# Kernel tuning notes

Measured on AMD Instinct MI355X. Metric: run time of the kernel, lower is better.

The kernel has to match this reference:

```python
import jax, jax.numpy as jnp
import numpy as np

H, W = 256, 512
SCORE_THR = 0.2
NMS_THR = 0.15
TOPK = 4096


def _make_anchors():
    xs = (np.arange(W) + 0.5) * 0.4 - 0.2 * W
    ys = (np.arange(H) + 0.5) * 0.4 - 0.2 * H
    gx, gy = np.meshgrid(xs, ys)            # [H, W]
    anc = np.zeros((H, W, 2, 7), dtype=np.float32)
    anc[..., 0] = gx[..., None]
    anc[..., 1] = gy[..., None]
    anc[..., 2] = -1.0
    anc[..., 3] = 1.56  # h
    anc[..., 4] = 1.6   # w
    anc[..., 5] = 3.9   # l
    anc[..., 0, 6] = 0.0
    anc[..., 1, 6] = np.pi / 2
    return jnp.asarray(anc)


def _make_T(theta, tx, ty, tz):
    c, s = np.cos(theta), np.sin(theta)
    T = np.eye(4, dtype=np.float32)
    T[0, 0], T[0, 1], T[1, 0], T[1, 1] = c, -s, s, c
    T[0, 3], T[1, 3], T[2, 3] = tx, ty, tz
    return jnp.asarray(T)


def setup_inputs() -> dict:
    key = jax.random.key(0)
    k1, k2, k3, k4 = jax.random.split(key, 4)
    return {
        "anchors": _make_anchors(),
        "psm_v": jax.random.normal(k1, (1, 2, H, W), jnp.float32),
        "rm_v": jax.random.normal(k2, (1, 14, H, W), jnp.float32) * 0.1,
        "psm_i": jax.random.normal(k3, (1, 2, H, W), jnp.float32),
        "rm_i": jax.random.normal(k4, (1, 14, H, W), jnp.float32) * 0.1,
        "t_proj": _make_T(0.05, 2.0, -1.0, 0.1),
        "t_ego": _make_T(-0.1, 5.0, 3.0, 0.0),
    }


def delta_to_boxes3d(rm, anchors):
    # rm: [1, 14, H, W] -> [A, 7]; anchors: [H, W, 2, 7] xyzhwlr -> [A, 7]
    d = jnp.transpose(rm[0], (1, 2, 0)).reshape(-1, 7)
    a = anchors.reshape(-1, 7)
    ad = jnp.sqrt(a[:, 4] ** 2 + a[:, 5] ** 2)          # diag of w,l
    xy = d[:, :2] * ad[:, None] + a[:, :2]
    z = d[:, 2] * a[:, 3] + a[:, 2]
    dims = jnp.exp(d[:, 3:6]) * a[:, 3:6]               # h, w, l
    yaw = d[:, 6] + a[:, 6]
    return jnp.concatenate([xy, z[:, None], dims, yaw[:, None]], axis=1)


def boxes_to_corners_3d(b):
    # b: [N, 7] x,y,z,h,w,l,yaw (order 'hwl') -> [N, 8, 3]
    h, w, l, yaw = b[:, 3], b[:, 4], b[:, 5], b[:, 6]
    sx = jnp.array([1, 1, -1, -1, 1, 1, -1, -1], jnp.float32) * 0.5
    sy = jnp.array([1, -1, -1, 1, 1, -1, -1, 1], jnp.float32) * 0.5
    sz = jnp.array([-1, -1, -1, -1, 1, 1, 1, 1], jnp.float32) * 0.5
    x = l[:, None] * sx
    y = w[:, None] * sy
    z = h[:, None] * sz
    c, s = jnp.cos(yaw)[:, None], jnp.sin(yaw)[:, None]
    xr = x * c - y * s + b[:, 0:1]
    yr = x * s + y * c + b[:, 1:2]
    zr = z + b[:, 2:3]
    return jnp.stack([xr, yr, zr], axis=-1)


def project_box3d(corners, T):
    # corners: [N, 8, 3]; T: [4, 4]
    return jnp.einsum('ij,nkj->nki', T[:3, :3], corners) + T[:3, 3]


def corner_to_center(corners):
    # inverse of boxes_to_corners_3d, order 'hwl'
    xyz = corners.mean(axis=1)
    h = corners[:, 4:, 2].mean(axis=1) - corners[:, :4, 2].mean(axis=1)
    dl = corners[:, (0, 1, 4, 5), :2] - corners[:, (3, 2, 7, 6), :2]
    dw = corners[:, (0, 3, 4, 7), :2] - corners[:, (1, 2, 5, 6), :2]
    l = jnp.linalg.norm(dl, axis=-1).mean(axis=1)
    w = jnp.linalg.norm(dw, axis=-1).mean(axis=1)
    d = dl.sum(axis=1)
    yaw = jnp.arctan2(d[:, 1], d[:, 0])
    return jnp.concatenate(
        [xyz, h[:, None], w[:, None], l[:, None], yaw[:, None]], axis=1)


def standup_boxes(corners):
    # [N, 8, 3] -> [N, 4] x1,y1,x2,y2 over BEV
    mn = corners[..., :2].min(axis=1)
    mx = corners[..., :2].max(axis=1)
    return jnp.concatenate([mn, mx], axis=1)


def iou_matrix(b):
    area = (b[:, 2] - b[:, 0]) * (b[:, 3] - b[:, 1])
    lt = jnp.maximum(b[:, None, :2], b[None, :, :2])
    rb = jnp.minimum(b[:, None, 2:], b[None, :, 2:])
    wh = jnp.clip(rb - lt, 0.0)
    inter = wh[..., 0] * wh[..., 1]
    return inter / (area[:, None] + area[None, :] - inter + 1e-6)


def nms_keep(iou, valid, thresh):
    K = iou.shape[0]
    idx = jnp.arange(K)

    def body(i, keep):
        sup = (iou[i] > thresh) & (idx > i) & keep[i]
        return keep & ~sup

    return jax.lax.fori_loop(0, K, body, valid)


def _branch(psm, rm, anchors):
    scores = jax.nn.sigmoid(jnp.transpose(psm[0], (1, 2, 0))).reshape(-1)
    boxes = delta_to_boxes3d(rm, anchors)
    return boxes, scores


def reference(anchors, psm_v, rm_v, psm_i, rm_i, t_proj, t_ego):
    boxes_v, scores_v = _branch(psm_v, rm_v, anchors)
    boxes_i, scores_i = _branch(psm_i, rm_i, anchors)
    # project infra branch boxes into ego frame via corner transform
    corners_i = boxes_to_corners_3d(boxes_i)
    boxes_i = corner_to_center(project_box3d(corners_i, t_proj))
    boxes = jnp.concatenate([boxes_v, boxes_i], axis=0)       # [2A, 7]
    scores = jnp.concatenate([scores_v, scores_i], axis=0)    # [2A]
    # project all to ego space
    proj = project_box3d(boxes_to_corners_3d(boxes), t_ego)   # [2A, 8, 3]
    # static replacement of masked_select: mask + top-K
    masked = jnp.where(scores > SCORE_THR, scores, -1.0)
    top_s, top_i = jax.lax.top_k(masked, TOPK)
    corners_k = proj[top_i]                                    # [K, 8, 3]
    iou = iou_matrix(standup_boxes(corners_k))
    keep = nms_keep(iou, top_s > SCORE_THR, NMS_THR)
    final = top_s * keep.astype(top_s.dtype)
    # pack corners + surviving scores: [K, 25]
    return jnp.concatenate([corners_k.reshape(TOPK, 24), final[:, None]], axis=1)
```

## Files before the change

kernel.cpp:

```cpp
#include <hip/hip_runtime.h>
#include <stdint.h>

typedef unsigned int u32;
typedef unsigned long long u64;

#define HH 256
#define WW 512
#define HW (HH*WW)
#define N2 (2*HW)
#define NT (2*N2)
#define TOPK 4096
#define SCORE_THR 0.2f
#define NMS_THR 0.15f

#define OFF_KEYS   0ull
#define OFF_GHIST  ((size_t)NT*4)
#define OFF_GHIST2 (OFF_GHIST + 4096)
#define OFF_CNT    (OFF_GHIST2 + 4096)
#define OFF_VALIDM (OFF_CNT + 16)
#define OFF_CAND   (OFF_VALIDM + 512)
#define OFF_STAND  OFF_CAND
#define OFF_SELIDX (OFF_CAND + 65536)
#define OFF_SELSC  (OFF_SELIDX + (size_t)TOPK*4)
#define OFF_TDIAG  (OFF_SELSC + (size_t)TOPK*4)
#define ZERO_BYTES (4096 + 4096 + 16)
#define RANK_J 8

#define SLOT8 4160

__device__ __forceinline__ u32 f2ord(float f) {
    u32 b = __float_as_uint(f);
    return (b & 0x80000000u) ? ~b : (b | 0x80000000u);
}

__global__ void __launch_bounds__(1024) k_keys(const float* __restrict__ psm_v,
                                               const float* __restrict__ psm_i,
                                               u32* __restrict__ keys,
                                               u32* __restrict__ ghist) {
    __shared__ u32 lh[1024];
    int t = threadIdx.x;
    lh[t] = 0;
    __syncthreads();
    int n = blockIdx.x * 1024 + t;
    int br = n >> 18;
    int m  = n & (N2 - 1);
    int a  = m & 1;
    int hw = m >> 1;
    const float* psm = br ? psm_i : psm_v;
    float x = psm[a * HW + hw];
    float s = 1.0f / (1.0f + __builtin_expf(-x));
    u32 key = 0u;
    if (s > SCORE_THR) key = f2ord(s);
    keys[n] = key;
    if (key) atomicAdd(&lh[key >> 22], 1u);
    __syncthreads();
    u32 c = lh[t];
    if (c) atomicAdd(&ghist[t], c);
}

__device__ __forceinline__ void pivot1024(const u32* __restrict__ arr, u32 target,
                                          u32* out_bin, u32* out_next, int l) {
    u32 h[16], loc[16];
#pragma unroll
    for (int j = 0; j < 16; ++j) h[j] = arr[l * 16 + j];
    loc[15] = h[15];
#pragma unroll
    for (int j = 14; j >= 0; --j) loc[j] = loc[j + 1] + h[j];
    u32 T = loc[0];
    u32 incl = T;
#pragma unroll
    for (int d = 1; d < 64; d <<= 1) {
        u32 v = __shfl_down(incl, d);
        if (l + d < 64) incl += v;
    }
    u32 E = incl - T;
#pragma unroll
    for (int j = 0; j < 16; ++j) {
        u32 S  = loc[j] + E;
        u32 Sn = (j < 15 ? loc[j + 1] : 0u) + E;
        if (S >= target && Sn < target) {
            *out_bin = (u32)(l * 16 + j);
            *out_next = Sn;
        }
    }
}

__global__ void __launch_bounds__(1024) k_hist2(const u32* __restrict__ ghist,
                                                const u32* __restrict__ keys,
                                                u32* __restrict__ ghist2) {
    __shared__ u32 lh[1024];
    __shared__ u32 b1_sh;
    int tid = threadIdx.x;
    lh[tid] = 0;
    if (tid < 64) {
        u32 bin = 0xFFFFFFFFu, nxt = 0;
        pivot1024(ghist, (u32)TOPK, &bin, &nxt, tid);
        if (bin != 0xFFFFFFFFu) b1_sh = bin;
    }
    __syncthreads();
    u32 b1 = b1_sh;
    int n = blockIdx.x * 1024 + tid;
    u32 key = keys[n];
    if ((key >> 22) == b1) atomicAdd(&lh[(key >> 12) & 1023u], 1u);
    __syncthreads();
    u32 c = lh[tid];
    if (c) atomicAdd(&ghist2[tid], c);
}

__global__ void __launch_bounds__(1024) k_collect(const u32* __restrict__ ghist,
                                                  const u32* __restrict__ ghist2,
                                                  const u32* __restrict__ keys,
                                                  u64* __restrict__ cand,
                                                  u32* __restrict__ cnt) {
    __shared__ u32 b1_sh, t2_sh, b2_sh;
    int tid = threadIdx.x;
    if (tid < 64) {
        u32 bin = 0xFFFFFFFFu, nxt = 0;
        pivot1024(ghist, (u32)TOPK, &bin, &nxt, tid);
        if (bin != 0xFFFFFFFFu) { b1_sh = bin; t2_sh = (u32)TOPK - nxt; }
    }
    __syncthreads();
    if (tid < 64) {
        u32 bin = 0xFFFFFFFFu, nxt = 0;
        pivot1024(ghist2, t2_sh, &bin, &nxt, tid);
        if (bin != 0xFFFFFFFFu) b2_sh = bin;
    }
    __syncthreads();
    u32 thr20 = (b1_sh << 10) | b2_sh;
    int n = blockIdx.x * 1024 + tid;
    u32 key = keys[n];
    if ((key >> 12) >= thr20) {
        u32 pos = atomicAdd(cnt, 1u);
        if (pos < 8192u)
            cand[pos] = ((u64)key << 32) | (u64)(u32)(~(u32)n);
    }
}

__global__ void __launch_bounds__(256) k_rank1(const u64* __restrict__ cand,
                                               const u32* __restrict__ cnt,
                                               u32* __restrict__ partial) {
    __shared__ u64 tile[1024];
    int tid = threadIdx.x;
    int i = blockIdx.x * 256 + tid;
    u32 base = blockIdx.y * 1024u;
    u32 c = *cnt;
    if (c > 8192u) c = 8192u;
    u64 my = (i < (int)c) ? cand[i] : 0ull;
#pragma unroll
    for (int k = 0; k < 4; ++k) {
        u32 idx = base + tid + k * 256;
        tile[tid + k * 256] = (idx < c) ? cand[idx] : 0ull;
    }
    __syncthreads();
    u32 lim = (c > base) ? ((c - base < 1024u) ? (c - base) : 1024u) : 0u;
    u32 r = 0;
#pragma unroll 4
    for (u32 k = 0; k < lim; ++k) r += (tile[k] > my) ? 1u : 0u;
    partial[blockIdx.y * 8192 + i] = r;
}

__global__ void __launch_bounds__(256) k_scatter(const u64* __restrict__ cand,
                                                 const u32* __restrict__ cnt,
                                                 const u32* __restrict__ partial,
                                                 u32* __restrict__ sel_idx) {
    int i = blockIdx.x * 256 + threadIdx.x;
    u32 c = *cnt;
    if (c > 8192u) c = 8192u;
    if (i >= (int)c) return;
    u32 rank = 0;
#pragma unroll
    for (int bj = 0; bj < RANK_J; ++bj) rank += partial[bj * 8192 + i];
    if (rank < (u32)TOPK) {
        u64 my = cand[i];
        sel_idx[rank] = ~((u32)(my & 0xFFFFFFFFull));
    }
}

__device__ __forceinline__ void box_corners(const float b[7], float cx[8], float cy[8], float cz[8]) {
    const float sx[8] = {0.5f,0.5f,-0.5f,-0.5f,0.5f,0.5f,-0.5f,-0.5f};
    const float sy[8] = {0.5f,-0.5f,-0.5f,0.5f,0.5f,-0.5f,-0.5f,0.5f};
    const float sz[8] = {-0.5f,-0.5f,-0.5f,-0.5f,0.5f,0.5f,0.5f,0.5f};
    float c = __builtin_cosf(b[6]), s = __builtin_sinf(b[6]);
#pragma unroll
    for (int k = 0; k < 8; k++) {
        float x = b[5] * sx[k], y = b[4] * sy[k], z = b[3] * sz[k];
        cx[k] = x * c - y * s + b[0];
        cy[k] = x * s + y * c + b[1];
        cz[k] = z + b[2];
    }
}

__device__ __forceinline__ void proj_T(const float* __restrict__ T, float cx[8], float cy[8], float cz[8]) {
#pragma unroll
    for (int k = 0; k < 8; k++) {
        float x = cx[k], y = cy[k], z = cz[k];
        cx[k] = T[0] * x + T[1] * y + T[2]  * z + T[3];
        cy[k] = T[4] * x + T[5] * y + T[6]  * z + T[7];
        cz[k] = T[8] * x + T[9] * y + T[10] * z + T[11];
    }
}

__device__ __forceinline__ void corner_to_center(const float cx[8], const float cy[8], const float cz[8], float b[7]) {
    float mx = 0.f, my = 0.f, mz = 0.f;
#pragma unroll
    for (int k = 0; k < 8; k++) { mx += cx[k]; my += cy[k]; mz += cz[k]; }
    mx *= 0.125f; my *= 0.125f; mz *= 0.125f;
    float htop = (cz[4] + cz[5] + cz[6] + cz[7]) * 0.25f;
    float hbot = (cz[0] + cz[1] + cz[2] + cz[3]) * 0.25f;
    const int lA[4] = {0,1,4,5}, lB[4] = {3,2,7,6};
    const int wA[4] = {0,3,4,7}, wB[4] = {1,2,5,6};
    float l = 0.f, w = 0.f, dx = 0.f, dy = 0.f;
#pragma unroll
    for (int i = 0; i < 4; i++) {
        float ax = cx[lA[i]] - cx[lB[i]];
        float ay = cy[lA[i]] - cy[lB[i]];
        l += __builtin_sqrtf(ax * ax + ay * ay);
        dx += ax; dy += ay;
    }
#pragma unroll
    for (int i = 0; i < 4; i++) {
        float ax = cx[wA[i]] - cx[wB[i]];
        float ay = cy[wA[i]] - cy[wB[i]];
        w += __builtin_sqrtf(ax * ax + ay * ay);
    }
    b[0] = mx; b[1] = my; b[2] = mz;
    b[3] = htop - hbot;
    b[4] = w * 0.25f;
    b[5] = l * 0.25f;
    b[6] = atan2f(dy, dx);
}

__global__ void __launch_bounds__(256) k_boxes(const float* __restrict__ anchors,
                                               const float* __restrict__ psm_v,
                                               const float* __restrict__ psm_i,
                                               const float* __restrict__ rm_v,
                                               const float* __restrict__ rm_i,
                                               const float* __restrict__ tproj,
                                               const float* __restrict__ tego,
                                               const u32* __restrict__ sel_idx,
                                               float* __restrict__ sel_sc,
                                               float* __restrict__ out,
                                               float4* __restrict__ stand,
                                               u64* __restrict__ validm) {
    int k = blockIdx.x * blockDim.x + threadIdx.x;
    if (k >= TOPK) return;
    int n = (int)(sel_idx[k] & (u32)(NT - 1));
    int br = n >> 18;
    int m  = n & (N2 - 1);
    int a  = m & 1;
    int hw = m >> 1;

    const float* psm = br ? psm_i : psm_v;
    float xs = psm[a * HW + hw];
    float s  = 1.0f / (1.0f + __builtin_expf(-xs));
    sel_sc[k] = (s > SCORE_THR) ? s : -1.0f;
    u64 vbits = __ballot(s > SCORE_THR);
    if ((threadIdx.x & 63) == 0) validm[k >> 6] = vbits;

    const float* rm = br ? rm_i : rm_v;
    float d[7];
#pragma unroll
    for (int j = 0; j < 7; j++) d[j] = rm[(a * 7 + j) * HW + hw];
    const float* anc = anchors + (size_t)m * 7;
    float a0 = anc[0], a1 = anc[1], a2 = anc[2], a3 = anc[3], a4 = anc[4], a5 = anc[5], a6 = anc[6];
    float ad = __builtin_sqrtf(a4 * a4 + a5 * a5);
    float b[7];
    b[0] = d[0] * ad + a0;
    b[1] = d[1] * ad + a1;
    b[2] = d[2] * a3 + a2;
    b[3] = __builtin_expf(d[3]) * a3;
    b[4] = __builtin_expf(d[4]) * a4;
    b[5] = __builtin_expf(d[5]) * a5;
    b[6] = d[6] + a6;

    if (br) {
        float cx[8], cy[8], cz[8];
        box_corners(b, cx, cy, cz);
        proj_T(tproj, cx, cy, cz);
        corner_to_center(cx, cy, cz, b);
    }

    float cx[8], cy[8], cz[8];
    box_corners(b, cx, cy, cz);
    proj_T(tego, cx, cy, cz);

    float mnx = cx[0], mny = cy[0], mxx = cx[0], mxy = cy[0];
#pragma unroll
    for (int c = 0; c < 8; c++) {
        out[(size_t)k * 25 + c * 3 + 0] = cx[c];
        out[(size_t)k * 25 + c * 3 + 1] = cy[c];
        out[(size_t)k * 25 + c * 3 + 2] = cz[c];
        mnx = fminf(mnx, cx[c]); mny = fminf(mny, cy[c]);
        mxx = fmaxf(mxx, cx[c]); mxy = fmaxf(mxy, cy[c]);
    }
    stand[k] = make_float4(mnx, mny, mxx, mxy);
}

__global__ void __launch_bounds__(256) k_mask(const float4* __restrict__ stand,
                                              u64* __restrict__ mask) {
    int i = blockIdx.x * 4 + (threadIdx.x >> 6);
    int t = threadIdx.x & 63;
    int w0 = i >> 6;
    float4 bi = stand[i];
    float areai = (bi.z - bi.x) * (bi.w - bi.y);
    u64 myword = 0ull;
    for (int w = w0; w < 64; ++w) {
        int j = w * 64 + t;
        float4 bj = stand[j];
        float areaj = (bj.z - bj.x) * (bj.w - bj.y);
        float ltx = fmaxf(bi.x, bj.x), lty = fmaxf(bi.y, bj.y);
        float rbx = fminf(bi.z, bj.z), rby = fminf(bi.w, bj.w);
        float iw = fmaxf(rbx - ltx, 0.0f), ih = fmaxf(rby - lty, 0.0f);
        float inter = iw * ih;
        float iou = inter / (areai + areaj - inter + 1e-6f);
        bool sup = (iou > NMS_THR) && (j > i);
        u64 bits = __ballot(sup);
        if (t == w) myword = bits;
    }
    mask[(size_t)i * 64 + t] = myword;
}

__global__ void __launch_bounds__(64) k_diag(const float4* __restrict__ stand,
                                             u64* __restrict__ tdiag) {
    __shared__ float4 sb[64];
    int B = blockIdx.x, l = threadIdx.x;
    float4 me = stand[B * 64 + l];
    sb[l] = me;
    __syncthreads();
    float aream = (me.z - me.x) * (me.w - me.y);
    u64 T = 0ull;
    for (int j = 0; j < 64; ++j) {
        float4 bj = sb[j];
        float areaj = (bj.z - bj.x) * (bj.w - bj.y);
        float ltx = fmaxf(bj.x, me.x), lty = fmaxf(bj.y, me.y);
        float rbx = fminf(bj.z, me.z), rby = fminf(bj.w, me.w);
        float iw = fmaxf(rbx - ltx, 0.0f), ih = fmaxf(rby - lty, 0.0f);
        float inter = iw * ih;
        float iou = inter / (areaj + aream - inter + 1e-6f);
        bool sup = (iou > NMS_THR) && (j < l);
        T |= sup ? (1ull << j) : 0ull;
    }
    tdiag[B * 64 + l] = T;
}

__device__ __forceinline__ u64 readlane64(u64 v, int lane) {
    u32 lo = (u32)__builtin_amdgcn_readlane((int)(u32)v, lane);
    u32 hi = (u32)__builtin_amdgcn_readlane((int)(u32)(v >> 32), lane);
    return ((u64)hi << 32) | (u64)lo;
}

__device__ __forceinline__ void nms_stage8(const u64* __restrict__ mask,
                                           const u64* __restrict__ tdiag,
                                           int c, int l, u64* wb) {
    bool act = (2 * (l & 31) + 1) >= c;
    const u64* gb = mask + (size_t)c * 4096 + (size_t)l * 2;
    if (act) {
#pragma unroll
        for (int k = 0; k < 32; ++k) {
            __builtin_amdgcn_global_load_lds(
                (const __attribute__((address_space(1))) void*)(gb + (size_t)k * 128),
                (__attribute__((address_space(3))) void*)(wb + (size_t)k * 128), 16, 0, 0);
        }
    }
    if (l < 32) {
        __builtin_amdgcn_global_load_lds(
            (const __attribute__((address_space(1))) void*)(tdiag + (size_t)c * 64 + (size_t)l * 2),
            (__attribute__((address_space(3))) void*)(wb + 4096), 16, 0, 0);
    }
}

__global__ void __launch_bounds__(64, 1)
k_nms(const u64* __restrict__ mask,
      const u64* __restrict__ tdiag,
      const u64* __restrict__ validm,
      const float* __restrict__ sc,
      float* __restrict__ out) {
    __shared__ u64 ring[3 * SLOT8];
    int l = threadIdx.x;
    u64 remv = 0ull;
    u64 keep = 0ull;
    u64 vreg = validm[l];

    nms_stage8(mask, tdiag, 0, l, ring);
    nms_stage8(mask, tdiag, 1, l, ring + SLOT8);

    for (int B = 0; B < 64; ++B) {
        int s = B % 3;
        u64* wb = ring + (size_t)s * SLOT8;
        if (B == 63) __builtin_amdgcn_s_waitcnt(0x0F70);
        else         __builtin_amdgcn_s_waitcnt(0x8F71);
        __builtin_amdgcn_sched_barrier(0);
        __asm__ volatile("" ::: "memory");
        u64 Tl = wb[4096 + l];
        if (B + 2 < 64)
            nms_stage8(mask, tdiag, B + 2, l, ring + (size_t)((B + 2) % 3) * SLOT8);
        u64 curw = readlane64(remv, B);
        u64 vm = readlane64(vreg, B);
        u64 ve = vm & ~curw;
        u64 D = 0ull, P = ve;
        while (D != P) {
            u64 nD = ve & ~__ballot((Tl & P) != 0ull);
            u64 nP = ve & ~__ballot((Tl & nD) != 0ull);
            D = nD; P = nP;
        }
        u64 kb = D;
        keep = (l == B) ? kb : keep;
        u32 klo = (u32)__builtin_amdgcn_readfirstlane((int)(u32)kb);
        u32 khi = (u32)__builtin_amdgcn_readfirstlane((int)(u32)(kb >> 32));
        u64 p = 0ull;
#pragma unroll
        for (int g = 0; g < 8; ++g) {
            u32 bits = ((g < 4 ? klo : khi) >> ((g & 3) * 8)) & 0xFFu;
            if (bits) {
#pragma unroll
                for (int k = 0; k < 8; ++k) {
                    u64 row = wb[(size_t)(g * 8 + k) * 64 + l];
                    p |= row & (0ull - (u64)((bits >> k) & 1u));
                }
            }
        }
        remv |= p;
    }

    for (int c = 0; c < 64; ++c) {
        u64 kc = readlane64(keep, c);
        float s = sc[c * 64 + l];
        out[(size_t)(c * 64 + l) * 25 + 24] = ((kc >> l) & 1ull) ? s : 0.0f;
    }
}

extern "C" void kernel_launch(void* const* d_in, const int* in_sizes, int n_in,
                              void* d_out, int out_size, void* d_ws, size_t ws_size,
                              hipStream_t stream) {
    const float* anchors = (const float*)d_in[0];
    const float* psm_v   = (const float*)d_in[1];
    const float* rm_v    = (const float*)d_in[2];
    const float* psm_i   = (const float*)d_in[3];
    const float* rm_i    = (const float*)d_in[4];
    const float* tproj   = (const float*)d_in[5];
    const float* tego    = (const float*)d_in[6];
    float* out = (float*)d_out;
    char* ws = (char*)d_ws;

    u32*    keys    = (u32*)(ws + OFF_KEYS);
    u64*    mask    = (u64*)(ws + OFF_KEYS);
    u32*    partial = (u32*)(ws + OFF_KEYS);
    u32*    ghist   = (u32*)(ws + OFF_GHIST);
    u32*    ghist2  = (u32*)(ws + OFF_GHIST2);
    u32*    cnt     = (u32*)(ws + OFF_CNT);
    u64*    validm  = (u64*)(ws + OFF_VALIDM);
    u64*    cand    = (u64*)(ws + OFF_CAND);
    float4* stand   = (float4*)(ws + OFF_STAND);
    u32*    sel_idx = (u32*)(ws + OFF_SELIDX);
    float*  sel_sc  = (float*)(ws + OFF_SELSC);
    u64*    tdiag   = (u64*)(ws + OFF_TDIAG);

    hipMemsetAsync(ws + OFF_GHIST, 0, ZERO_BYTES, stream);
    k_keys   <<<NT / 1024, 1024, 0, stream>>>(psm_v, psm_i, keys, ghist);
    k_hist2  <<<NT / 1024, 1024, 0, stream>>>(ghist, keys, ghist2);
    k_collect<<<NT / 1024, 1024, 0, stream>>>(ghist, ghist2, keys, cand, cnt);
    k_rank1  <<<dim3(32, RANK_J), 256, 0, stream>>>(cand, cnt, partial);
    k_scatter<<<32, 256, 0, stream>>>(cand, cnt, partial, sel_idx);
    k_boxes  <<<TOPK / 256, 256, 0, stream>>>(anchors, psm_v, psm_i, rm_v, rm_i,
                                              tproj, tego, sel_idx, sel_sc, out,
                                              stand, validm);
    k_mask   <<<TOPK / 4, 256, 0, stream>>>(stand, mask);
    k_diag   <<<64, 64, 0, stream>>>(stand, tdiag);
    k_nms    <<<1, 64, 0, stream>>>(mask, tdiag, validm, sel_sc, out);
}
```

Baseline: 287.7 us.

## Split serial NMS across 64 blocks with flag-based inter-block publishing

Replaces the single-wavefront NMS, which walked all 64 column blocks serially with an LDS prefetch ring, by 64 blocks, one per 64-box column block. Each block preloads its mask column into LDS, then spins on per-block keep words published in global memory by the earlier blocks. It ORs in their suppression, resolves its own diagonal block, and publishes its keep mask. This aims to overlap the mask loading across CUs and shorten the serial chain. The cost is cross-block spin-waiting on relaxed atomics, which relies on all 64 blocks being resident at once and on the published values becoming visible without fences.

```diff
diff --git a/kernel.cpp b/kernel.cpp
--- a/kernel.cpp
+++ b/kernel.cpp
@@ -17,16 +17,15 @@
 #define OFF_GHIST  ((size_t)NT*4)
 #define OFF_GHIST2 (OFF_GHIST + 4096)
 #define OFF_CNT    (OFF_GHIST2 + 4096)
-#define OFF_VALIDM (OFF_CNT + 16)
+#define OFF_PUB    (OFF_CNT + 16)
+#define OFF_VALIDM (OFF_PUB + 2048)
 #define OFF_CAND   (OFF_VALIDM + 512)
 #define OFF_STAND  OFF_CAND
 #define OFF_SELIDX (OFF_CAND + 65536)
 #define OFF_SELSC  (OFF_SELIDX + (size_t)TOPK*4)
 #define OFF_TDIAG  (OFF_SELSC + (size_t)TOPK*4)
-#define ZERO_BYTES (4096 + 4096 + 16)
+#define ZERO_BYTES (4096 + 4096 + 16 + 2048)
 #define RANK_J 8
-
-#define SLOT8 4160
 
 __device__ __forceinline__ u32 f2ord(float f) {
     u32 b = __float_as_uint(f);
@@ -349,84 +348,75 @@
     return ((u64)hi << 32) | (u64)lo;
 }
 
-__device__ __forceinline__ void nms_stage8(const u64* __restrict__ mask,
-                                           const u64* __restrict__ tdiag,
-                                           int c, int l, u64* wb) {
-    bool act = (2 * (l & 31) + 1) >= c;
-    const u64* gb = mask + (size_t)c * 4096 + (size_t)l * 2;
-    if (act) {
-#pragma unroll
-        for (int k = 0; k < 32; ++k) {
-            __builtin_amdgcn_global_load_lds(
-                (const __attribute__((address_space(1))) void*)(gb + (size_t)k * 128),
-                (__attribute__((address_space(3))) void*)(wb + (size_t)k * 128), 16, 0, 0);
-        }
-    }
-    if (l < 32) {
-        __builtin_amdgcn_global_load_lds(
-            (const __attribute__((address_space(1))) void*)(tdiag + (size_t)c * 64 + (size_t)l * 2),
-            (__attribute__((address_space(3))) void*)(wb + 4096), 16, 0, 0);
-    }
-}
-
 __global__ void __launch_bounds__(64, 1)
 k_nms(const u64* __restrict__ mask,
       const u64* __restrict__ tdiag,
       const u64* __restrict__ validm,
       const float* __restrict__ sc,
+      u64* pub,
       float* __restrict__ out) {
-    __shared__ u64 ring[3 * SLOT8];
+    __shared__ u64 colbuf[4032];
+    int bid = blockIdx.x;
+    int c = ((bid & 7) << 3) | (bid >> 3);
     int l = threadIdx.x;
-    u64 remv = 0ull;
-    u64 keep = 0ull;
-    u64 vreg = validm[l];
-
-    nms_stage8(mask, tdiag, 0, l, ring);
-    nms_stage8(mask, tdiag, 1, l, ring + SLOT8);
-
-    for (int B = 0; B < 64; ++B) {
-        int s = B % 3;
-        u64* wb = ring + (size_t)s * SLOT8;
-        if (B == 63) __builtin_amdgcn_s_waitcnt(0x0F70);
-        else         __builtin_amdgcn_s_waitcnt(0x8F71);
-        __builtin_amdgcn_sched_barrier(0);
-        __asm__ volatile("" ::: "memory");
-        u64 Tl = wb[4096 + l];
-        if (B + 2 < 64)
-            nms_stage8(mask, tdiag, B + 2, l, ring + (size_t)((B + 2) % 3) * SLOT8);
-        u64 curw = readlane64(remv, B);
-        u64 vm = readlane64(vreg, B);
-        u64 ve = vm & ~curw;
-        u64 D = 0ull, P = ve;
-        while (D != P) {
-            u64 nD = ve & ~__ballot((Tl & P) != 0ull);
-            u64 nP = ve & ~__ballot((Tl & nD) != 0ull);
-            D = nD; P = nP;
+    u64 Tl = tdiag[c * 64 + l];
+    u64 vm = validm[c];
+
+    for (int p0 = 0; p0 < c; p0 += 8) {
+        u64 w[8];
+        int nb = (c - p0 < 8) ? (c - p0) : 8;
+        for (int k = 0; k < nb; ++k)
+            w[k] = mask[((size_t)((p0 + k) * 64 + l)) * 64 + (size_t)c];
+        for (int k = 0; k < nb; ++k)
+            colbuf[(p0 + k) * 64 + l] = w[k];
+    }
+
+    u64 acc = 0;
+    int p = 0;
+    while (p < c) {
+        int idx = 2 * p + l;
+        u64 v = __hip_atomic_load(&pub[idx], __ATOMIC_RELAXED,
+                                  __HIP_MEMORY_SCOPE_AGENT);
+        bool ok = ((u32)v == (u32)(p + (l >> 1) + 1)) && (p + (l >> 1) < c);
+        u64 bal = __ballot(ok);
+        u64 bad = ~(bal & (bal >> 1)) & 0x5555555555555555ull;
+        int t = (bad == 0ull) ? 32 : (__builtin_ctzll(bad) >> 1);
+        if (t > c - p) t = c - p;
+        for (int q = 0; q < t; ++q) {
+            u64 va = readlane64(v, 2 * q);
+            u64 vb = readlane64(v, 2 * q + 1);
+            u64 kb = (va >> 32) | ((vb >> 32) << 32);
+            u64 w = colbuf[(p + q) * 64 + l];
+            acc |= w & (0ull - ((kb >> l) & 1ull));
         }
-        u64 kb = D;
-        keep = (l == B) ? kb : keep;
-        u32 klo = (u32)__builtin_amdgcn_readfirstlane((int)(u32)kb);
-        u32 khi = (u32)__builtin_amdgcn_readfirstlane((int)(u32)(kb >> 32));
-        u64 p = 0ull;
-#pragma unroll
-        for (int g = 0; g < 8; ++g) {
-            u32 bits = ((g < 4 ? klo : khi) >> ((g & 3) * 8)) & 0xFFu;
-            if (bits) {
-#pragma unroll
-                for (int k = 0; k < 8; ++k) {
-                    u64 row = wb[(size_t)(g * 8 + k) * 64 + l];
-                    p |= row & (0ull - (u64)((bits >> k) & 1u));
-                }
-            }
-        }
-        remv |= p;
-    }
-
-    for (int c = 0; c < 64; ++c) {
-        u64 kc = readlane64(keep, c);
-        float s = sc[c * 64 + l];
-        out[(size_t)(c * 64 + l) * 25 + 24] = ((kc >> l) & 1ull) ? s : 0.0f;
-    }
+        p += t;
+        if (t == 0) __builtin_amdgcn_s_sleep(1);
+    }
+
+#pragma unroll
+    for (int d = 1; d < 64; d <<= 1)
+        acc |= (u64)__shfl_xor((unsigned long long)acc, d);
+
+    u64 ve = vm & ~acc;
+    u64 D = 0ull, P = ve;
+    while (D != P) {
+        u64 nD = ve & ~__ballot((Tl & P) != 0ull);
+        u64 nP = ve & ~__ballot((Tl & nD) != 0ull);
+        D = nD; P = nP;
+    }
+    u64 kb = D;
+
+    if (l == 0) {
+        __hip_atomic_store(&pub[2 * c],
+                           (((u64)(u32)kb) << 32) | (u64)(u32)(c + 1),
+                           __ATOMIC_RELAXED, __HIP_MEMORY_SCOPE_AGENT);
+        __hip_atomic_store(&pub[2 * c + 1],
+                           (((u64)(u32)(kb >> 32)) << 32) | (u64)(u32)(c + 1),
+                           __ATOMIC_RELAXED, __HIP_MEMORY_SCOPE_AGENT);
+    }
+
+    float s = sc[c * 64 + l];
+    out[(size_t)(c * 64 + l) * 25 + 24] = ((kb >> l) & 1ull) ? s : 0.0f;
 }
 
 extern "C" void kernel_launch(void* const* d_in, const int* in_sizes, int n_in,
@@ -448,6 +438,7 @@
     u32*    ghist   = (u32*)(ws + OFF_GHIST);
     u32*    ghist2  = (u32*)(ws + OFF_GHIST2);
     u32*    cnt     = (u32*)(ws + OFF_CNT);
+    u64*    pub     = (u64*)(ws + OFF_PUB);
     u64*    validm  = (u64*)(ws + OFF_VALIDM);
     u64*    cand    = (u64*)(ws + OFF_CAND);
     float4* stand   = (float4*)(ws + OFF_STAND);
@@ -466,5 +457,5 @@
                                               stand, validm);
     k_mask   <<<TOPK / 4, 256, 0, stream>>>(stand, mask);
     k_diag   <<<64, 64, 0, stream>>>(stand, tdiag);
-    k_nms    <<<1, 64, 0, stream>>>(mask, tdiag, validm, sel_sc, out);
-}
+    k_nms    <<<64, 64, 0, stream>>>(mask, tdiag, validm, sel_sc, pub, out);
+}
```

After: 251.1 us. 12.7% less time.
